# Kernel tuning notes

Measured on AMD Instinct MI355X. Metric: run time of the kernel, lower is better.

Reference implementation:

```python
import jax, jax.numpy as jnp
import numpy as np

ALPHAS = (0.1, 0.3, 0.5)
WEIGHTS = (0.5, 0.3, 0.2)

B, T, D = 32, 8192, 64


def setup_inputs() -> dict:
    key = jax.random.key(0)
    k1, k2 = jax.random.split(key)
    pred = jax.random.normal(k1, (B, T, D), dtype=jnp.float32)
    target = jax.random.normal(k2, (B, T, D), dtype=jnp.float32)
    return {"pred": pred, "target": target}


def _ema(x, alpha):
    # ema_0 = x_0 ; ema_i = alpha*x_i + (1-alpha)*ema_{i-1}
    # Express each step as affine op (mult, add) and compose with an
    # associative scan along the time axis (dim=1):  y_i = mult*y_{i-1} + add.
    mult = jnp.full(x.shape, 1.0 - alpha, dtype=x.dtype).at[:, 0].set(0.0)
    add = (alpha * x).at[:, 0].set(x[:, 0])

    def combine(c1, c2):  # apply c1 first, then c2
        a1, b1 = c1
        a2, b2 = c2
        return (a1 * a2, b1 * a2 + b2)

    _, ema = jax.lax.associative_scan(combine, (mult, add), axis=1)
    return ema


def _scale_loss(pred, target, alpha):
    pe = _ema(pred, alpha)   # [B, T, D]
    te = _ema(target, alpha)
    pd = pe[:, 1:] - pe[:, :-1]
    td = te[:, 1:] - te[:, :-1]
    mismatch = jnp.sign(pd) != jnp.sign(td)
    step_err = jnp.square(pe[:, 1:] - te[:, 1:])
    masked = jnp.where(mismatch, step_err, jnp.zeros_like(step_err))
    return masked.mean(axis=1)  # [B, D]


def reference(pred, target):
    loss = sum(w * _scale_loss(pred, target, a) for a, w in zip(ALPHAS, WEIGHTS))
    return loss.mean()  # reduction='mean'
```

## Files before the change

### kernel.cpp

```cpp
#include <hip/hip_runtime.h>


namespace {
constexpr int BB  = 32;
constexpr int TT  = 8192;
constexpr int DD  = 64;
constexpr int CH  = 64;
constexpr int WU  = 32;
constexpr int NCH = TT / CH;
constexpr int WPB = 4;
constexpr int BT  = 16;
constexpr float INV_NORM = 1.0f / (8191.0f * 2048.0f);
}

__global__ void zero_out_kernel(float* o) { o[0] = 0.0f; }

__device__ __forceinline__ void load16(const float* __restrict__ p,
                                       const float* __restrict__ q, int bt,
                                       float (&xs)[BT], float (&ys)[BT]) {
#pragma unroll
  for (int i = 0; i < BT; ++i) {
    xs[i] = p[(bt + i) * DD];
    ys[i] = q[(bt + i) * DD];
  }
}

__device__ __forceinline__ void warm16_a0(const float (&xs)[BT], const float (&ys)[BT],
                                          float& pe0, float& te0) {
#pragma unroll
  for (int i = 0; i < BT; ++i) {
    pe0 = fmaf(0.1f, xs[i] - pe0, pe0);
    te0 = fmaf(0.1f, ys[i] - te0, te0);
  }
}

__device__ __forceinline__ void warm16_all(const float (&xs)[BT], const float (&ys)[BT],
    float& pe0, float& te0, float& pe1, float& te1, float& pe2, float& te2) {
#pragma unroll
  for (int i = 0; i < BT; ++i) {
    pe0 = fmaf(0.1f, xs[i] - pe0, pe0);  te0 = fmaf(0.1f, ys[i] - te0, te0);
    pe1 = fmaf(0.3f, xs[i] - pe1, pe1);  te1 = fmaf(0.3f, ys[i] - te1, te1);
    pe2 = fmaf(0.5f, xs[i] - pe2, pe2);  te2 = fmaf(0.5f, ys[i] - te2, te2);
  }
}

__device__ __forceinline__ void step1(float xx, float yy, float a, float w,
                                      float& pe, float& te, float& acc) {
  float dx = xx - pe;
  float dy = yy - te;
  pe = fmaf(a, dx, pe);
  te = fmaf(a, dy, te);
  float e   = pe - te;
  float sel = (dx * dy < 0.0f) ? w : 0.0f;
  acc = fmaf(sel, e * e, acc);
}

__device__ __forceinline__ void acc16_all(const float (&xs)[BT], const float (&ys)[BT],
    float& pe0, float& te0, float& pe1, float& te1, float& pe2, float& te2,
    float& acc) {
#pragma unroll
  for (int i = 0; i < BT; ++i) {
    step1(xs[i], ys[i], 0.1f, 0.5f, pe0, te0, acc);
    step1(xs[i], ys[i], 0.3f, 0.3f, pe1, te1, acc);
    step1(xs[i], ys[i], 0.5f, 0.2f, pe2, te2, acc);
  }
}

__global__ __launch_bounds__(256, 4) void ms_trend_loss_kernel(
    const float* __restrict__ pred, const float* __restrict__ targ,
    float* __restrict__ out) {
  const int lane = threadIdx.x & 63;
  const int wave = threadIdx.x >> 6;
  const int unit = blockIdx.x * WPB + wave;
  const int b = unit >> 7;
  const int c = unit & 127;
  const int s = c * CH;
  const int start = (c == 0) ? 0 : (s - WU);

  const float* p = pred + (b * TT + start) * DD + lane;
  const float* q = targ + (b * TT + start) * DD + lane;

  float pe0, pe1, pe2, te0, te1, te2;
  float acc = 0.0f;
  float xa[BT], ya[BT], xb[BT], yb[BT], xc[BT], yc[BT];

  if (c == 0) {
    load16(p, q, 0, xa, ya);
    load16(p, q, BT, xb, yb);
    load16(p, q, 2 * BT, xc, yc);
    __builtin_amdgcn_sched_barrier(0);
    pe0 = pe1 = pe2 = xa[0];
    te0 = te1 = te2 = ya[0];
    acc16_all(xa, ya, pe0, te0, pe1, te1, pe2, te2, acc);
    load16(p, q, 3 * BT, xa, ya);
    __builtin_amdgcn_sched_barrier(0);
    acc16_all(xb, yb, pe0, te0, pe1, te1, pe2, te2, acc);
    acc16_all(xc, yc, pe0, te0, pe1, te1, pe2, te2, acc);
    acc16_all(xa, ya, pe0, te0, pe1, te1, pe2, te2, acc);
  } else {
    load16(p, q, 0, xa, ya);
    load16(p, q, BT, xb, yb);
    load16(p, q, 2 * BT, xc, yc);
    __builtin_amdgcn_sched_barrier(0);
    pe0 = xa[0];
    te0 = ya[0];
    warm16_a0(xa, ya, pe0, te0);
    load16(p, q, 3 * BT, xa, ya);
    __builtin_amdgcn_sched_barrier(0);
    pe1 = pe2 = xb[0];
    te1 = te2 = yb[0];
    warm16_all(xb, yb, pe0, te0, pe1, te1, pe2, te2);
    load16(p, q, 4 * BT, xb, yb);
    __builtin_amdgcn_sched_barrier(0);
    acc16_all(xc, yc, pe0, te0, pe1, te1, pe2, te2, acc);
    load16(p, q, 5 * BT, xc, yc);
    __builtin_amdgcn_sched_barrier(0);
    acc16_all(xa, ya, pe0, te0, pe1, te1, pe2, te2, acc);
    acc16_all(xb, yb, pe0, te0, pe1, te1, pe2, te2, acc);
    acc16_all(xc, yc, pe0, te0, pe1, te1, pe2, te2, acc);
  }

#pragma unroll
  for (int off = 32; off > 0; off >>= 1) acc += __shfl_down(acc, off);
  __shared__ float sred[WPB];
  if (lane == 0) sred[wave] = acc;
  __syncthreads();
  if (threadIdx.x == 0) {
    float t = sred[0] + sred[1] + sred[2] + sred[3];
    atomicAdd(out, t * INV_NORM);
  }
}

extern "C" void kernel_launch(void* const* d_in, const int* in_sizes, int n_in,
                              void* d_out, int out_size, void* d_ws, size_t ws_size,
                              hipStream_t stream) {
  (void)in_sizes; (void)n_in; (void)out_size; (void)d_ws; (void)ws_size;
  const float* pred = (const float*)d_in[0];
  const float* targ = (const float*)d_in[1];
  float* out = (float*)d_out;

  zero_out_kernel<<<1, 1, 0, stream>>>(out);
  ms_trend_loss_kernel<<<BB * NCH / WPB, 256, 0, stream>>>(pred, targ, out);
}
```

Baseline: 154.5 us.

## Load inputs as float4 and transpose through per-wave LDS staging buffers

Replaces per-lane scalar strided global loads with float4 vector loads across 4 rows per instruction, then stages the tile into per-wave shared memory so each lane can read its own column serially. The goal is fewer global load instructions and wider memory transactions. In exchange it adds LDS writes and reads per element and 32KB of shared memory per block, which may limit occupancy. It also switches the occupancy hint to amdgpu_waves_per_eu(4,4).

```diff
diff --git a/kernel.cpp b/kernel.cpp
--- a/kernel.cpp
+++ b/kernel.cpp
@@ -15,32 +15,46 @@
 
 __global__ void zero_out_kernel(float* o) { o[0] = 0.0f; }
 
-__device__ __forceinline__ void load16(const float* __restrict__ p,
-                                       const float* __restrict__ q, int bt,
-                                       float (&xs)[BT], float (&ys)[BT]) {
+__device__ __forceinline__ void gload(const float* __restrict__ pv,
+                                      const float* __restrict__ qv, int bt,
+                                      float4 (&rx)[4], float4 (&ry)[4]) {
 #pragma unroll
-  for (int i = 0; i < BT; ++i) {
-    xs[i] = p[(bt + i) * DD];
-    ys[i] = q[(bt + i) * DD];
+  for (int j = 0; j < 4; ++j) {
+    rx[j] = *reinterpret_cast<const float4*>(pv + (bt + 4 * j) * DD);
+    ry[j] = *reinterpret_cast<const float4*>(qv + (bt + 4 * j) * DD);
   }
 }
 
-__device__ __forceinline__ void warm16_a0(const float (&xs)[BT], const float (&ys)[BT],
-                                          float& pe0, float& te0) {
+__device__ __forceinline__ void stage(float* __restrict__ lx,
+                                      float* __restrict__ ly,
+                                      const float4 (&rx)[4], const float4 (&ry)[4]) {
 #pragma unroll
-  for (int i = 0; i < BT; ++i) {
-    pe0 = fmaf(0.1f, xs[i] - pe0, pe0);
-    te0 = fmaf(0.1f, ys[i] - te0, te0);
+  for (int j = 0; j < 4; ++j) {
+    *reinterpret_cast<float4*>(lx + 4 * j * DD) = rx[j];
+    *reinterpret_cast<float4*>(ly + 4 * j * DD) = ry[j];
   }
 }
 
-__device__ __forceinline__ void warm16_all(const float (&xs)[BT], const float (&ys)[BT],
+__device__ __forceinline__ void warm16_a0_t(const float* __restrict__ tx,
+                                            const float* __restrict__ ty,
+                                            float& pe0, float& te0) {
+#pragma unroll
+  for (int i = 0; i < BT; ++i) {
+    float xx = tx[i * DD], yy = ty[i * DD];
+    pe0 = fmaf(0.1f, xx - pe0, pe0);
+    te0 = fmaf(0.1f, yy - te0, te0);
+  }
+}
+
+__device__ __forceinline__ void warm16_all_t(const float* __restrict__ tx,
+    const float* __restrict__ ty,
     float& pe0, float& te0, float& pe1, float& te1, float& pe2, float& te2) {
 #pragma unroll
   for (int i = 0; i < BT; ++i) {
-    pe0 = fmaf(0.1f, xs[i] - pe0, pe0);  te0 = fmaf(0.1f, ys[i] - te0, te0);
-    pe1 = fmaf(0.3f, xs[i] - pe1, pe1);  te1 = fmaf(0.3f, ys[i] - te1, te1);
-    pe2 = fmaf(0.5f, xs[i] - pe2, pe2);  te2 = fmaf(0.5f, ys[i] - te2, te2);
+    float xx = tx[i * DD], yy = ty[i * DD];
+    pe0 = fmaf(0.1f, xx - pe0, pe0);  te0 = fmaf(0.1f, yy - te0, te0);
+    pe1 = fmaf(0.3f, xx - pe1, pe1);  te1 = fmaf(0.3f, yy - te1, te1);
+    pe2 = fmaf(0.5f, xx - pe2, pe2);  te2 = fmaf(0.5f, yy - te2, te2);
   }
 }
 
@@ -55,20 +69,24 @@
   acc = fmaf(sel, e * e, acc);
 }
 
-__device__ __forceinline__ void acc16_all(const float (&xs)[BT], const float (&ys)[BT],
+__device__ __forceinline__ void acc16_t(const float* __restrict__ tx,
+    const float* __restrict__ ty,
     float& pe0, float& te0, float& pe1, float& te1, float& pe2, float& te2,
     float& acc) {
 #pragma unroll
   for (int i = 0; i < BT; ++i) {
-    step1(xs[i], ys[i], 0.1f, 0.5f, pe0, te0, acc);
-    step1(xs[i], ys[i], 0.3f, 0.3f, pe1, te1, acc);
-    step1(xs[i], ys[i], 0.5f, 0.2f, pe2, te2, acc);
+    float xx = tx[i * DD], yy = ty[i * DD];
+    step1(xx, yy, 0.1f, 0.5f, pe0, te0, acc);
+    step1(xx, yy, 0.3f, 0.3f, pe1, te1, acc);
+    step1(xx, yy, 0.5f, 0.2f, pe2, te2, acc);
   }
 }
 
-__global__ __launch_bounds__(256, 4) void ms_trend_loss_kernel(
-    const float* __restrict__ pred, const float* __restrict__ targ,
-    float* __restrict__ out) {
+__global__ void __launch_bounds__(256)
+__attribute__((amdgpu_waves_per_eu(4, 4)))
+ms_trend_loss_kernel(const float* __restrict__ pred,
+                     const float* __restrict__ targ,
+                     float* __restrict__ out) {
   const int lane = threadIdx.x & 63;
   const int wave = threadIdx.x >> 6;
   const int unit = blockIdx.x * WPB + wave;
@@ -77,47 +95,69 @@
   const int s = c * CH;
   const int start = (c == 0) ? 0 : (s - WU);
 
-  const float* p = pred + (b * TT + start) * DD + lane;
-  const float* q = targ + (b * TT + start) * DD + lane;
+  const int rsub = lane >> 4;
+  const int csub = (lane & 15) * 4;
+
+  const float* pv = pred + (b * TT + start) * DD + rsub * DD + csub;
+  const float* qv = targ + (b * TT + start) * DD + rsub * DD + csub;
+
+  __shared__ float lds_x[WPB][BT * DD];
+  __shared__ float lds_y[WPB][BT * DD];
+  float* lxw = &lds_x[wave][rsub * DD + csub];
+  float* lyw = &lds_y[wave][rsub * DD + csub];
+  const float* txr = &lds_x[wave][lane];
+  const float* tyr = &lds_y[wave][lane];
 
   float pe0, pe1, pe2, te0, te1, te2;
   float acc = 0.0f;
-  float xa[BT], ya[BT], xb[BT], yb[BT], xc[BT], yc[BT];
+  float4 ax[4], ay[4], bx[4], by[4];
 
   if (c == 0) {
-    load16(p, q, 0, xa, ya);
-    load16(p, q, BT, xb, yb);
-    load16(p, q, 2 * BT, xc, yc);
+    gload(pv, qv, 0, ax, ay);
+    gload(pv, qv, BT, bx, by);
     __builtin_amdgcn_sched_barrier(0);
-    pe0 = pe1 = pe2 = xa[0];
-    te0 = te1 = te2 = ya[0];
-    acc16_all(xa, ya, pe0, te0, pe1, te1, pe2, te2, acc);
-    load16(p, q, 3 * BT, xa, ya);
+    stage(lxw, lyw, ax, ay);
+    gload(pv, qv, 2 * BT, ax, ay);
     __builtin_amdgcn_sched_barrier(0);
-    acc16_all(xb, yb, pe0, te0, pe1, te1, pe2, te2, acc);
-    acc16_all(xc, yc, pe0, te0, pe1, te1, pe2, te2, acc);
-    acc16_all(xa, ya, pe0, te0, pe1, te1, pe2, te2, acc);
+    pe0 = pe1 = pe2 = txr[0];
+    te0 = te1 = te2 = tyr[0];
+    acc16_t(txr, tyr, pe0, te0, pe1, te1, pe2, te2, acc);
+    stage(lxw, lyw, bx, by);
+    gload(pv, qv, 3 * BT, bx, by);
+    __builtin_amdgcn_sched_barrier(0);
+    acc16_t(txr, tyr, pe0, te0, pe1, te1, pe2, te2, acc);
+    stage(lxw, lyw, ax, ay);
+    acc16_t(txr, tyr, pe0, te0, pe1, te1, pe2, te2, acc);
+    stage(lxw, lyw, bx, by);
+    acc16_t(txr, tyr, pe0, te0, pe1, te1, pe2, te2, acc);
   } else {
-    load16(p, q, 0, xa, ya);
-    load16(p, q, BT, xb, yb);
-    load16(p, q, 2 * BT, xc, yc);
+    gload(pv, qv, 0, ax, ay);
+    gload(pv, qv, BT, bx, by);
     __builtin_amdgcn_sched_barrier(0);
-    pe0 = xa[0];
-    te0 = ya[0];
-    warm16_a0(xa, ya, pe0, te0);
-    load16(p, q, 3 * BT, xa, ya);
+    stage(lxw, lyw, ax, ay);
+    gload(pv, qv, 2 * BT, ax, ay);
     __builtin_amdgcn_sched_barrier(0);
-    pe1 = pe2 = xb[0];
-    te1 = te2 = yb[0];
-    warm16_all(xb, yb, pe0, te0, pe1, te1, pe2, te2);
-    load16(p, q, 4 * BT, xb, yb);
+    pe0 = txr[0];
+    te0 = tyr[0];
+    warm16_a0_t(txr, tyr, pe0, te0);
+    stage(lxw, lyw, bx, by);
+    gload(pv, qv, 3 * BT, bx, by);
     __builtin_amdgcn_sched_barrier(0);
-    acc16_all(xc, yc, pe0, te0, pe1, te1, pe2, te2, acc);
-    load16(p, q, 5 * BT, xc, yc);
+    pe1 = pe2 = txr[0];
+    te1 = te2 = tyr[0];
+    warm16_all_t(txr, tyr, pe0, te0, pe1, te1, pe2, te2);
+    stage(lxw, lyw, ax, ay);
+    gload(pv, qv, 4 * BT, ax, ay);
     __builtin_amdgcn_sched_barrier(0);
-    acc16_all(xa, ya, pe0, te0, pe1, te1, pe2, te2, acc);
-    acc16_all(xb, yb, pe0, te0, pe1, te1, pe2, te2, acc);
-    acc16_all(xc, yc, pe0, te0, pe1, te1, pe2, te2, acc);
+    acc16_t(txr, tyr, pe0, te0, pe1, te1, pe2, te2, acc);
+    stage(lxw, lyw, bx, by);
+    gload(pv, qv, 5 * BT, bx, by);
+    __builtin_amdgcn_sched_barrier(0);
+    acc16_t(txr, tyr, pe0, te0, pe1, te1, pe2, te2, acc);
+    stage(lxw, lyw, ax, ay);
+    acc16_t(txr, tyr, pe0, te0, pe1, te1, pe2, te2, acc);
+    stage(lxw, lyw, bx, by);
+    acc16_t(txr, tyr, pe0, te0, pe1, te1, pe2, te2, acc);
   }
 
 #pragma unroll
```

Result: faster. 151.2 us (-2.1%).
